# Kernel optimization log

Hardware: AMD Instinct MI355X
Metric: run time of the kernel (lower is better)

The kernel has to match this reference:

```python
import math
import jax, jax.numpy as jnp
import numpy as np

HEADS = 16
MASKED_BIAS = -10000.0


def setup_inputs() -> dict:
    key = jax.random.key(0)
    kq, kk, kv = jax.random.split(key, 3)
    B, S, D = 4, 1024, 2048
    q = jax.random.normal(kq, (B, S, D), dtype=jnp.float32)
    k = jax.random.normal(kk, (B, S, D), dtype=jnp.float32)
    v = jax.random.normal(kv, (B, S, D), dtype=jnp.float32)
    return {"q": q, "k": k, "v": v}


def _mha(q, k, v):
    B, Sq, D = q.shape
    Sk = k.shape[-2]
    hd = D // HEADS
    # (B, H, S, hd)
    qh = q.reshape(B, Sq, HEADS, hd).transpose(0, 2, 1, 3)
    kh = k.reshape(B, Sk, HEADS, hd).transpose(0, 2, 1, 3)
    vh = v.reshape(B, Sk, HEADS, hd).transpose(0, 2, 1, 3)
    scores = jnp.einsum("bhqd,bhkd->bhqk", qh, kh) / math.sqrt(hd)
    # causal mask: query i attends to keys <= i (aligned to end of kv)
    qi = jnp.arange(Sq)[:, None] + (Sk - Sq)
    ki = jnp.arange(Sk)[None, :]
    causal = ki <= qi  # (Sq, Sk)
    scores = jnp.where(causal[None, None], scores, jnp.asarray(MASKED_BIAS, scores.dtype))
    attn = jax.nn.softmax(scores, axis=-1)
    out = jnp.einsum("bhqk,bhkd->bhqd", attn, vh)
    return out.transpose(0, 2, 1, 3).reshape(B, Sq, D)


def reference(q, k, v):
    return _mha(q, k, v)
```

## Files before the change

### kernel.cpp

```cpp
#include <hip/hip_runtime.h>
#include <hip/hip_bf16.h>


#define HEADS  16
#define HD     128
#define SEQ    1024
#define DMODEL 2048

typedef _Float16 f16;
typedef __attribute__((ext_vector_type(8))) _Float16 f16x8;
typedef __attribute__((ext_vector_type(4))) _Float16 f16x4;
typedef __attribute__((ext_vector_type(4))) float    f32x4;
typedef __attribute__((ext_vector_type(4))) unsigned int u32x4;

__device__ __forceinline__ unsigned int pkrtz(float a, float b) {
    return __builtin_bit_cast(unsigned int, __builtin_amdgcn_cvt_pkrtz(a, b));
}

__global__ __launch_bounds__(256, 2)
void fa_fwd(const float* __restrict__ Q,
            const float* __restrict__ K,
            const float* __restrict__ V,
            float* __restrict__ O)
{
    __shared__ f16 kT[64 * 128];
    __shared__ f16 vT[128 * 64];

    const int tid  = threadIdx.x;
    const int lane = tid & 63;
    const int wv   = tid >> 6;
    const int quad = lane >> 4;
    const int cl   = lane & 15;

    const int bh = blockIdx.x;
    const int qt = 15 - blockIdx.y;
    const int qb = qt * 64;
    const long long head_off = ((long long)(bh >> 4) * SEQ) * DMODEL
                             + (long long)(bh & 15) * HD;
    const float rscale = 0.08838834764831845f;

    const int krow = tid >> 4;
    const int kg   = tid & 15;
    const int kgs  = kg ^ krow;
    const int vr0  = (tid & 31) * 2;
    const int vcg  = tid >> 5;
    const int vg   = vr0 >> 3;
    const int vo   = vr0 & 7;

    f32x4 kraw[8], vraw[8];

    auto loadKV = [&](int kbase) {
        #pragma unroll
        for (int i = 0; i < 4; ++i) {
            const float* kp = K + head_off + (long long)(kbase + krow + i * 16) * DMODEL + kg * 8;
            kraw[2 * i]     = *(const f32x4*)kp;
            kraw[2 * i + 1] = *(const f32x4*)(kp + 4);
        }
        const float* vp = V + head_off + (long long)(kbase + vr0) * DMODEL + vcg * 16;
        #pragma unroll
        for (int j = 0; j < 4; ++j) {
            vraw[j]     = *(const f32x4*)(vp + 4 * j);
            vraw[4 + j] = *(const f32x4*)(vp + DMODEL + 4 * j);
        }
    };

    const int qrow = qb + wv * 16 + cl;
    f16x8 qf[4];
    {
        const float* qp = Q + head_off + (long long)qrow * DMODEL + quad * 8;
        #pragma unroll
        for (int kk = 0; kk < 4; ++kk) {
            f32x4 qa = *(const f32x4*)(qp + kk * 32);
            f32x4 qc = *(const f32x4*)(qp + kk * 32 + 4);
            union { f16x8 v; unsigned int u[4]; } qw;
            qw.u[0] = pkrtz(qa[0], qa[1]);
            qw.u[1] = pkrtz(qa[2], qa[3]);
            qw.u[2] = pkrtz(qc[0], qc[1]);
            qw.u[3] = pkrtz(qc[2], qc[3]);
            qf[kk] = qw.v;
        }
    }

    f32x4 acc[8];
    #pragma unroll
    for (int i = 0; i < 8; ++i) acc[i] = (f32x4){0.f, 0.f, 0.f, 0.f};
    float ls = 0.f;

    loadKV(0);

    #pragma unroll 1
    for (int kt = 0; kt <= qt; ++kt) {
        __syncthreads();

        #pragma unroll
        for (int i = 0; i < 4; ++i) {
            u32x4 w;
            w.x = pkrtz(kraw[2 * i][0], kraw[2 * i][1]);
            w.y = pkrtz(kraw[2 * i][2], kraw[2 * i][3]);
            w.z = pkrtz(kraw[2 * i + 1][0], kraw[2 * i + 1][1]);
            w.w = pkrtz(kraw[2 * i + 1][2], kraw[2 * i + 1][3]);
            *(u32x4*)&kT[(krow + 16 * i) * 128 + kgs * 8] = w;
        }
        #pragma unroll
        for (int j = 0; j < 16; ++j) {
            unsigned int pk = pkrtz(vraw[j >> 2][j & 3], vraw[4 + (j >> 2)][j & 3]);
            *(unsigned int*)&vT[(vcg * 16 + j) * 64 + ((vg ^ (j & 7)) * 8) + vo] = pk;
        }
        __syncthreads();

        if (kt < qt) loadKV((kt + 1) * 64);

        f32x4 sc[4];
        #pragma unroll
        for (int st = 0; st < 4; ++st) sc[st] = (f32x4){0.f, 0.f, 0.f, 0.f};
        #pragma unroll
        for (int kk = 0; kk < 4; ++kk) {
            #pragma unroll
            for (int st = 0; st < 4; ++st) {
                f16x8 kf = *(const f16x8*)&kT[(st * 16 + cl) * 128
                                              + ((kk * 4 + quad) ^ cl) * 8];
                sc[st] = __builtin_amdgcn_mfma_f32_16x16x32_f16(kf, qf[kk], sc[st], 0, 0, 0);
            }
        }

        const int kbase = kt * 64;
        f16x4 pf[4];
        if (kt == qt) {
            #pragma unroll
            for (int st = 0; st < 4; ++st) {
                float e[4];
                #pragma unroll
                for (int r = 0; r < 4; ++r) {
                    int key = kbase + st * 16 + quad * 4 + r;
                    float ex = __expf(sc[st][r] * rscale);
                    e[r] = (key <= qrow) ? ex : 0.f;
                    ls += e[r];
                }
                union { f16x4 v; unsigned int u[2]; } pw;
                pw.u[0] = pkrtz(e[0], e[1]);
                pw.u[1] = pkrtz(e[2], e[3]);
                pf[st] = pw.v;
            }
        } else {
            #pragma unroll
            for (int st = 0; st < 4; ++st) {
                float e[4];
                #pragma unroll
                for (int r = 0; r < 4; ++r) {
                    e[r] = __expf(sc[st][r] * rscale);
                    ls += e[r];
                }
                union { f16x4 v; unsigned int u[2]; } pw;
                pw.u[0] = pkrtz(e[0], e[1]);
                pw.u[1] = pkrtz(e[2], e[3]);
                pf[st] = pw.v;
            }
        }

        #pragma unroll
        for (int dt = 0; dt < 8; ++dt) {
            #pragma unroll
            for (int st = 0; st < 4; ++st) {
                f16x4 vf = *(const f16x4*)&vT[(dt * 16 + cl) * 64
                                              + ((st * 2 + (quad >> 1)) ^ (cl & 7)) * 8
                                              + (quad & 1) * 4];
                acc[dt] = __builtin_amdgcn_mfma_f32_16x16x16f16(vf, pf[st], acc[dt], 0, 0, 0);
            }
        }
    }

    float lsum = ls;
    lsum += __shfl_xor(lsum, 16, 64);
    lsum += __shfl_xor(lsum, 32, 64);
    const float rl = 1.0f / lsum;

    float* op = O + head_off + (long long)qrow * DMODEL + quad * 4;
    #pragma unroll
    for (int dt = 0; dt < 8; ++dt) {
        f32x4 o4 = acc[dt];
        o4[0] *= rl; o4[1] *= rl; o4[2] *= rl; o4[3] *= rl;
        *(f32x4*)(op + dt * 16) = o4;
    }
}

extern "C" void kernel_launch(void* const* d_in, const int* in_sizes, int n_in,
                              void* d_out, int out_size, void* d_ws, size_t ws_size,
                              hipStream_t stream) {
    const float* q = (const float*)d_in[0];
    const float* k = (const float*)d_in[1];
    const float* v = (const float*)d_in[2];
    float* o = (float*)d_out;

    dim3 grid(4 * HEADS, SEQ / 64);
    dim3 block(256);
    fa_fwd<<<grid, block, 0, stream>>>(q, k, v, o);
}
```

Measured before the change: 169.7 us.

## Pair causal query tiles per block to balance work and share K/V loads

```diff
diff --git a/kernel.cpp b/kernel.cpp
--- a/kernel.cpp
+++ b/kernel.cpp
@@ -17,7 +17,7 @@
     return __builtin_bit_cast(unsigned int, __builtin_amdgcn_cvt_pkrtz(a, b));
 }
 
-__global__ __launch_bounds__(256, 2)
+__global__ __launch_bounds__(512, 4)
 void fa_fwd(const float* __restrict__ Q,
             const float* __restrict__ K,
             const float* __restrict__ V,
@@ -31,40 +31,46 @@
     const int wv   = tid >> 6;
     const int quad = lane >> 4;
     const int cl   = lane & 15;
+    const int tileSel = wv >> 2;
+    const int w4   = wv & 3;
 
     const int bh = blockIdx.x;
-    const int qt = 15 - blockIdx.y;
-    const int qb = qt * 64;
+    const int y  = blockIdx.y;
+    const int a  = (y < 4) ? y : 11 - y;
+    const int myqt  = tileSel ? (15 - a) : a;
+    const int qb    = myqt * 64;
+    const int ktmax = 15 - a;
+
     const long long head_off = ((long long)(bh >> 4) * SEQ) * DMODEL
                              + (long long)(bh & 15) * HD;
     const float rscale = 0.08838834764831845f;
 
     const int krow = tid >> 4;
     const int kg   = tid & 15;
-    const int kgs  = kg ^ krow;
+    const int kgs  = kg ^ (krow & 15);
     const int vr0  = (tid & 31) * 2;
     const int vcg  = tid >> 5;
     const int vg   = vr0 >> 3;
     const int vo   = vr0 & 7;
 
-    f32x4 kraw[8], vraw[8];
+    f32x4 kraw[4], vraw[4];
 
     auto loadKV = [&](int kbase) {
         #pragma unroll
-        for (int i = 0; i < 4; ++i) {
-            const float* kp = K + head_off + (long long)(kbase + krow + i * 16) * DMODEL + kg * 8;
+        for (int i = 0; i < 2; ++i) {
+            const float* kp = K + head_off
+                            + (long long)(kbase + krow + 32 * i) * DMODEL + kg * 8;
             kraw[2 * i]     = *(const f32x4*)kp;
             kraw[2 * i + 1] = *(const f32x4*)(kp + 4);
         }
-        const float* vp = V + head_off + (long long)(kbase + vr0) * DMODEL + vcg * 16;
-        #pragma unroll
-        for (int j = 0; j < 4; ++j) {
-            vraw[j]     = *(const f32x4*)(vp + 4 * j);
-            vraw[4 + j] = *(const f32x4*)(vp + DMODEL + 4 * j);
-        }
+        const float* vp = V + head_off + (long long)(kbase + vr0) * DMODEL + vcg * 8;
+        vraw[0] = *(const f32x4*)(vp);
+        vraw[1] = *(const f32x4*)(vp + 4);
+        vraw[2] = *(const f32x4*)(vp + DMODEL);
+        vraw[3] = *(const f32x4*)(vp + DMODEL + 4);
     };
 
-    const int qrow = qb + wv * 16 + cl;
+    const int qrow = qb + w4 * 16 + cl;
     f16x8 qf[4];
     {
         const float* qp = Q + head_off + (long long)qrow * DMODEL + quad * 8;
@@ -89,82 +95,84 @@
     loadKV(0);
 
     #pragma unroll 1
-    for (int kt = 0; kt <= qt; ++kt) {
+    for (int kt = 0; kt <= ktmax; ++kt) {
         __syncthreads();
 
         #pragma unroll
-        for (int i = 0; i < 4; ++i) {
+        for (int i = 0; i < 2; ++i) {
             u32x4 w;
             w.x = pkrtz(kraw[2 * i][0], kraw[2 * i][1]);
             w.y = pkrtz(kraw[2 * i][2], kraw[2 * i][3]);
             w.z = pkrtz(kraw[2 * i + 1][0], kraw[2 * i + 1][1]);
             w.w = pkrtz(kraw[2 * i + 1][2], kraw[2 * i + 1][3]);
-            *(u32x4*)&kT[(krow + 16 * i) * 128 + kgs * 8] = w;
-        }
-        #pragma unroll
-        for (int j = 0; j < 16; ++j) {
-            unsigned int pk = pkrtz(vraw[j >> 2][j & 3], vraw[4 + (j >> 2)][j & 3]);
-            *(unsigned int*)&vT[(vcg * 16 + j) * 64 + ((vg ^ (j & 7)) * 8) + vo] = pk;
+            *(u32x4*)&kT[(krow + 32 * i) * 128 + kgs * 8] = w;
+        }
+        #pragma unroll
+        for (int j = 0; j < 8; ++j) {
+            unsigned int pk = pkrtz(vraw[j >> 2][j & 3], vraw[2 + (j >> 2)][j & 3]);
+            *(unsigned int*)&vT[(vcg * 8 + j) * 64 + ((vg ^ j) * 8) + vo] = pk;
         }
         __syncthreads();
 
-        if (kt < qt) loadKV((kt + 1) * 64);
-
-        f32x4 sc[4];
-        #pragma unroll
-        for (int st = 0; st < 4; ++st) sc[st] = (f32x4){0.f, 0.f, 0.f, 0.f};
-        #pragma unroll
-        for (int kk = 0; kk < 4; ++kk) {
+        if (kt < ktmax) loadKV((kt + 1) * 64);
+
+        if (kt <= myqt) {
+            f32x4 sc[4];
             #pragma unroll
-            for (int st = 0; st < 4; ++st) {
-                f16x8 kf = *(const f16x8*)&kT[(st * 16 + cl) * 128
-                                              + ((kk * 4 + quad) ^ cl) * 8];
-                sc[st] = __builtin_amdgcn_mfma_f32_16x16x32_f16(kf, qf[kk], sc[st], 0, 0, 0);
+            for (int st = 0; st < 4; ++st) sc[st] = (f32x4){0.f, 0.f, 0.f, 0.f};
+            #pragma unroll
+            for (int kk = 0; kk < 4; ++kk) {
+                #pragma unroll
+                for (int st = 0; st < 4; ++st) {
+                    f16x8 kf = *(const f16x8*)&kT[(st * 16 + cl) * 128
+                                                  + ((kk * 4 + quad) ^ cl) * 8];
+                    sc[st] = __builtin_amdgcn_mfma_f32_16x16x32_f16(kf, qf[kk], sc[st], 0, 0, 0);
+                }
             }
-        }
-
-        const int kbase = kt * 64;
-        f16x4 pf[4];
-        if (kt == qt) {
+
+            const int kbase = kt * 64;
+            f16x4 pf[4];
+            if (kt == myqt) {
+                #pragma unroll
+                for (int st = 0; st < 4; ++st) {
+                    float e[4];
+                    #pragma unroll
+                    for (int r = 0; r < 4; ++r) {
+                        int key = kbase + st * 16 + quad * 4 + r;
+                        float ex = __expf(sc[st][r] * rscale);
+                        e[r] = (key <= qrow) ? ex : 0.f;
+                        ls += e[r];
+                    }
+                    union { f16x4 v; unsigned int u[2]; } pw;
+                    pw.u[0] = pkrtz(e[0], e[1]);
+                    pw.u[1] = pkrtz(e[2], e[3]);
+                    pf[st] = pw.v;
+                }
+            } else {
+                #pragma unroll
+                for (int st = 0; st < 4; ++st) {
+                    float e[4];
+                    #pragma unroll
+                    for (int r = 0; r < 4; ++r) {
+                        e[r] = __expf(sc[st][r] * rscale);
+                        ls += e[r];
+                    }
+                    union { f16x4 v; unsigned int u[2]; } pw;
+                    pw.u[0] = pkrtz(e[0], e[1]);
+                    pw.u[1] = pkrtz(e[2], e[3]);
+                    pf[st] = pw.v;
+                }
+            }
+
             #pragma unroll
-            for (int st = 0; st < 4; ++st) {
-                float e[4];
-                #pragma unroll
-                for (int r = 0; r < 4; ++r) {
-                    int key = kbase + st * 16 + quad * 4 + r;
-                    float ex = __expf(sc[st][r] * rscale);
-                    e[r] = (key <= qrow) ? ex : 0.f;
-                    ls += e[r];
-                }
-                union { f16x4 v; unsigned int u[2]; } pw;
-                pw.u[0] = pkrtz(e[0], e[1]);
-                pw.u[1] = pkrtz(e[2], e[3]);
-                pf[st] = pw.v;
-            }
-        } else {
-            #pragma unroll
-            for (int st = 0; st < 4; ++st) {
-                float e[4];
-                #pragma unroll
-                for (int r = 0; r < 4; ++r) {
-                    e[r] = __expf(sc[st][r] * rscale);
-                    ls += e[r];
-                }
-                union { f16x4 v; unsigned int u[2]; } pw;
-                pw.u[0] = pkrtz(e[0], e[1]);
-                pw.u[1] = pkrtz(e[2], e[3]);
-                pf[st] = pw.v;
-            }
-        }
-
-        #pragma unroll
-        for (int dt = 0; dt < 8; ++dt) {
-            #pragma unroll
-            for (int st = 0; st < 4; ++st) {
-                f16x4 vf = *(const f16x4*)&vT[(dt * 16 + cl) * 64
-                                              + ((st * 2 + (quad >> 1)) ^ (cl & 7)) * 8
-                                              + (quad & 1) * 4];
-                acc[dt] = __builtin_amdgcn_mfma_f32_16x16x16f16(vf, pf[st], acc[dt], 0, 0, 0);
+            for (int dt = 0; dt < 8; ++dt) {
+                #pragma unroll
+                for (int st = 0; st < 4; ++st) {
+                    f16x4 vf = *(const f16x4*)&vT[(dt * 16 + cl) * 64
+                                                  + ((st * 2 + (quad >> 1)) ^ (cl & 7)) * 8
+                                                  + (quad & 1) * 4];
+                    acc[dt] = __builtin_amdgcn_mfma_f32_16x16x16f16(vf, pf[st], acc[dt], 0, 0, 0);
+                }
             }
         }
     }
@@ -191,7 +199,7 @@
     const float* v = (const float*)d_in[2];
     float* o = (float*)d_out;
 
-    dim3 grid(4 * HEADS, SEQ / 64);
-    dim3 block(256);
+    dim3 grid(4 * HEADS, 8);
+    dim3 block(512);
     fa_fwd<<<grid, block, 0, stream>>>(q, k, v, o);
 }
```

Measured after the change: 176.4 us. 1.04x slower.
